# Optimization experiments

Measured on AMD Instinct MI355X. Metric: run time of the kernel, lower is better.

Reference implementation:

```python
import jax, jax.numpy as jnp
import numpy as np

B, S, D = 4, 2048, 1024      # batch, seq, d_model
H = 4096                     # expert hidden_size
E, K = 8, 2                  # num_experts, top_k
Z_COEF, BAL_COEF = 0.001, 0.01


def setup_inputs() -> dict:
    key = jax.random.key(0)
    ks = jax.random.split(key, 10)
    sc = 0.02
    return {
        "x": jax.random.normal(ks[0], (B, S, D), jnp.float32),
        "gate_w": jax.random.normal(ks[1], (D, E), jnp.float32) * sc,
        "keys_w": jax.random.normal(ks[2], (E, D, H), jnp.float32) * sc,
        "keys_b": jnp.zeros((E, H), jnp.float32),
        "values_w": jax.random.normal(ks[3], (E, H, D), jnp.float32) * sc,
        "values_b": jnp.zeros((E, D), jnp.float32),
        "shared_keys_w": jax.random.normal(ks[4], (D, H), jnp.float32) * sc,
        "shared_keys_b": jnp.zeros((H,), jnp.float32),
        "shared_values_w": jax.random.normal(ks[5], (H, D), jnp.float32) * sc,
        "shared_values_b": jnp.zeros((D,), jnp.float32),
    }


def reference(x, gate_w, keys_w, keys_b, values_w, values_b,
              shared_keys_w, shared_keys_b, shared_values_w, shared_values_b):
    b, s, d = x.shape
    xf = x.reshape(-1, d)                                  # [N, D]

    # ---- Router (top-k, softmax over selected scores) ----
    logits = xf @ gate_w                                   # [N, E]
    scores, idx = jax.lax.top_k(logits, K)                 # [N, K]
    w = jax.nn.softmax(scores, axis=-1)                    # [N, K]

    # Aux losses (training path)
    one_hot = jax.nn.one_hot(idx, E, dtype=w.dtype)        # [N, K, E]
    usage = (one_hot * w[..., None]).sum(axis=(0, 1))      # [E]
    balance_loss = usage.std() / usage.mean() * BAL_COEF
    z_loss = jnp.square(jax.nn.logsumexp(logits, axis=-1)).mean() * Z_COEF
    router_loss = balance_loss + z_loss

    # ---- Shared expert(s): single FFN, divided by count (=1) ----
    out = jax.nn.gelu(xf @ shared_keys_w + shared_keys_b) @ shared_values_w + shared_values_b

    # ---- Training path: dense per-expert FFN, masked combine ----
    # hidden: [N, E, H]
    hidden = jax.nn.gelu(jnp.einsum('nd,edh->neh', xf, keys_w) + keys_b)
    expert_out = jnp.einsum('neh,ehd->ned', hidden, values_w) + values_b  # [N, E, D]
    comb = (one_hot * w[..., None]).sum(axis=1)            # [N, E] per-token expert weight
    out = out + jnp.einsum('ned,ne->nd', expert_out, comb)

    return out.reshape(b, s, d), router_loss
```

## Files before the change

kernel.cpp:

```cpp
#include <hip/hip_runtime.h>
#include <hip/hip_bf16.h>


#define N_TOK 8192
#define DM    1024
#define HD    4096
#define NE    8
#define NKTOT 16384
#define PERM_CAP 17408
#define MAX_TILES 136
#define BAND 17
#define RTOK_BLK 16

typedef __attribute__((ext_vector_type(8))) short bhalf8;
typedef __attribute__((ext_vector_type(4))) float floatx4;

__device__ __forceinline__ unsigned short f2bf(float f) {
  union { float f; unsigned int u; } v; v.f = f;
  unsigned int u = v.u;
  return (unsigned short)((u + 0x7fffu + ((u >> 16) & 1u)) >> 16);
}

__device__ __forceinline__ float bf2f(unsigned short h) {
  union { unsigned int u; float f; } v; v.u = ((unsigned int)h) << 16;
  return v.f;
}

__device__ __forceinline__ float gelu_tanh(float h) {
  float u = 0.7978845608028654f * (h + 0.044715f * h * h * h);
  float t = 1.0f - 2.0f / (1.0f + __expf(2.0f * u));
  return 0.5f * h * (1.0f + t);
}

__device__ __forceinline__ void gload16(const unsigned short* g, void* l) {
  __builtin_amdgcn_global_load_lds(
      (const __attribute__((address_space(1))) void*)g,
      (__attribute__((address_space(3))) void*)l, 16, 0, 0);
}

__global__ void init_kernel(int* perm, float* permw, float* usage, float* zsum,
                            int* counts, int* fill) {
  int i = blockIdx.x * 256 + threadIdx.x;
  if (i < PERM_CAP) { perm[i] = 0; permw[i] = 0.0f; }
  if (i < NE) { usage[i] = 0.0f; counts[i] = 0; fill[i] = 0; }
  if (i == 0) zsum[0] = 0.0f;
}

__global__ void cvt_x_kernel(const float* __restrict__ x, unsigned short* __restrict__ xb) {
  size_t i = (size_t)(blockIdx.x * 256 + threadIdx.x) * 4;
  float4 v = *(const float4*)(x + i);
  ushort4 o;
  o.x = f2bf(v.x); o.y = f2bf(v.y); o.z = f2bf(v.z); o.w = f2bf(v.w);
  *(ushort4*)(xb + i) = o;
}

__global__ void router_kernel(const float* __restrict__ x, const float* __restrict__ gw,
                              int* __restrict__ idxb, float* __restrict__ wbuf,
                              float* __restrict__ usage, float* __restrict__ zsum,
                              int* __restrict__ counts) {
  __shared__ float s_use[NE];
  __shared__ int   s_cnt[NE];
  __shared__ float s_z;
  int t = threadIdx.x;
  if (t < NE) { s_use[t] = 0.0f; s_cnt[t] = 0; }
  if (t == 0) s_z = 0.0f;
  __syncthreads();

  int wave = t >> 6;
  int lane = t & 63;

  float luse[NE]; int lcnt[NE];
#pragma unroll
  for (int e = 0; e < NE; e++) { luse[e] = 0.0f; lcnt[e] = 0; }
  float lz = 0.0f;

#pragma unroll
  for (int i = 0; i < 4; i++) {
    int n = blockIdx.x * RTOK_BLK + wave * 4 + i;
    const float* xr = x + (size_t)n * DM;
    float acc[NE];
#pragma unroll
    for (int e = 0; e < NE; e++) acc[e] = 0.0f;
    for (int d = lane; d < DM; d += 64) {
      float xv = xr[d];
      const float* g = gw + (size_t)d * NE;
#pragma unroll
      for (int e = 0; e < NE; e++) acc[e] += xv * g[e];
    }
#pragma unroll
    for (int e = 0; e < NE; e++) {
#pragma unroll
      for (int off = 32; off > 0; off >>= 1) acc[e] += __shfl_xor(acc[e], off);
    }
    if (lane == 0) {
      float m1 = acc[0]; int i1 = 0;
#pragma unroll
      for (int e = 1; e < NE; e++) if (acc[e] > m1) { m1 = acc[e]; i1 = e; }
      float m2 = -3.0e38f; int i2 = 0;
#pragma unroll
      for (int e = 0; e < NE; e++) if (e != i1 && acc[e] > m2) { m2 = acc[e]; i2 = e; }
      float e1 = __expf(m2 - m1);
      float w1 = 1.0f / (1.0f + e1);
      float w2 = e1 / (1.0f + e1);
      float s = 0.0f;
#pragma unroll
      for (int e = 0; e < NE; e++) s += __expf(acc[e] - m1);
      float lse = m1 + __logf(s);
      idxb[n * 2 + 0] = i1; idxb[n * 2 + 1] = i2;
      wbuf[n * 2 + 0] = w1; wbuf[n * 2 + 1] = w2;
      luse[i1] += w1; luse[i2] += w2;
      lcnt[i1]++;     lcnt[i2]++;
      lz += lse * lse;
    }
  }

  if (lane == 0) {
#pragma unroll
    for (int e = 0; e < NE; e++) {
      atomicAdd(&s_use[e], luse[e]);
      atomicAdd(&s_cnt[e], lcnt[e]);
    }
    atomicAdd(&s_z, lz);
  }
  __syncthreads();
  if (t < NE) {
    atomicAdd(&usage[t], s_use[t]);
    atomicAdd(&counts[t], s_cnt[t]);
  }
  if (t == 0) atomicAdd(zsum, s_z);
}

__global__ void scan_kernel(const int* __restrict__ counts, int* __restrict__ poff,
                            int* __restrict__ tileE, int* __restrict__ tileR,
                            int* __restrict__ nTiles,
                            const float* __restrict__ usage, const float* __restrict__ zsum,
                            float* __restrict__ lossOut) {
  if (threadIdx.x == 0 && blockIdx.x == 0) {
    int run = 0, nt = 0;
    for (int e = 0; e < NE; e++) {
      poff[e] = run;
      int t = (counts[e] + 127) >> 7;
      for (int i = 0; i < t; i++) { tileE[nt] = e; tileR[nt] = run + i * 128; nt++; }
      run += t << 7;
    }
    *nTiles = nt;
    float mean = 0.0f;
    for (int e = 0; e < NE; e++) mean += usage[e];
    mean *= (1.0f / NE);
    float var = 0.0f;
    for (int e = 0; e < NE; e++) { float d = usage[e] - mean; var += d * d; }
    var *= (1.0f / NE);
    float bal = sqrtf(var) / mean * 0.01f;
    float z = (zsum[0] / (float)N_TOK) * 0.001f;
    lossOut[0] = bal + z;
  }
}

__global__ void scatter_kernel(const int* __restrict__ idxb, const float* __restrict__ wbuf,
                               const int* __restrict__ poff, int* __restrict__ fill,
                               int* __restrict__ perm, float* __restrict__ permw,
                               int* __restrict__ pos) {
  __shared__ int lcnt[NE];
  __shared__ int lbase[NE];
  int t = threadIdx.x;
  if (t < NE) lcnt[t] = 0;
  __syncthreads();
  int i = blockIdx.x * 256 + t;
  int e = idxb[i];
  int r = atomicAdd(&lcnt[e], 1);
  __syncthreads();
  if (t < NE) lbase[t] = atomicAdd(&fill[t], lcnt[t]);
  __syncthreads();
  int p = poff[e] + lbase[e] + r;
  perm[p] = i >> 1;
  permw[p] = wbuf[i];
  pos[i] = p;
}

__global__ void transpose_cvt_kernel(const float* __restrict__ src,
                                     unsigned short* __restrict__ dst, int R, int C) {
  __shared__ float tile[64][65];
  size_t bo = (size_t)blockIdx.z * R * C;
  src += bo; dst += bo;
  int r0 = blockIdx.x * 64, c0 = blockIdx.y * 64;
  int c = threadIdx.x & 63, r = threadIdx.x >> 6;
#pragma unroll
  for (int i = 0; i < 16; i++)
    tile[r + i * 4][c] = src[(size_t)(r0 + r + i * 4) * C + c0 + c];
  __syncthreads();
#pragma unroll
  for (int i = 0; i < 16; i++) {
    int oc = r + i * 4;
    float v = tile[c][oc];
    dst[(size_t)(c0 + oc) * R + r0 + c] = f2bf(v);
  }
}

__global__ void combine_kernel(float* __restrict__ out,
                               const unsigned short* __restrict__ eout,
                               const int* __restrict__ pos) {
  int t = blockIdx.x;
  int d = threadIdx.x * 8;
  int p0 = pos[t * 2], p1 = pos[t * 2 + 1];
  float* o = out + (size_t)t * DM + d;
  const unsigned short* e0 = eout + (size_t)p0 * DM + d;
  const unsigned short* e1 = eout + (size_t)p1 * DM + d;
  float4 a = *(const float4*)(o);
  float4 b = *(const float4*)(o + 4);
  ushort4 u0a = *(const ushort4*)(e0), u0b = *(const ushort4*)(e0 + 4);
  ushort4 u1a = *(const ushort4*)(e1), u1b = *(const ushort4*)(e1 + 4);
  a.x += bf2f(u0a.x) + bf2f(u1a.x);
  a.y += bf2f(u0a.y) + bf2f(u1a.y);
  a.z += bf2f(u0a.z) + bf2f(u1a.z);
  a.w += bf2f(u0a.w) + bf2f(u1a.w);
  b.x += bf2f(u0b.x) + bf2f(u1b.x);
  b.y += bf2f(u0b.y) + bf2f(u1b.y);
  b.z += bf2f(u0b.z) + bf2f(u1b.z);
  b.w += bf2f(u0b.w) + bf2f(u1b.w);
  *(float4*)(o) = a;
  *(float4*)(o + 4) = b;
}

template<int MODE>
__device__ __forceinline__ void gemm_body(
    const unsigned short* __restrict__ A,
    const unsigned short* __restrict__ BT,
    const float* __restrict__ bias,
    float* __restrict__ outF,
    unsigned short* __restrict__ outH,
    int Kd, int Nd,
    const int* __restrict__ perm,
    const float* __restrict__ permw,
    const int* __restrict__ tileE,
    const int* __restrict__ tileR,
    const int* __restrict__ nTiles) {
  __shared__ __align__(16) unsigned short As[128 * 64];
  __shared__ __align__(16) unsigned short Bs[128 * 64];

  int id = blockIdx.x;
  int xcd = id & 7, q = id >> 3;
  int mt, ntile;
  if (MODE == 0) {
    mt = xcd * 8 + (q & 7);
    ntile = q >> 3;
  } else if (MODE == 1) {
    ntile = q & 7;
    mt = xcd * 8 + (q >> 3);
  } else if (MODE == 2) {
    int n_in = q & 7, m_in = (q >> 3) & 3, ng = (q >> 5) & 3, mg = q >> 7;
    int mband = mg * 4 + m_in;
    if (mband >= BAND) return;
    mt = xcd * BAND + mband;
    ntile = ng * 8 + n_in;
  } else {
    mt = xcd * BAND + (q >> 3);
    ntile = q & 7;
  }

  int n0 = ntile * 128;
  int prow0 = 0, m0 = 0;
  if (MODE >= 2) {
    if (mt >= *nTiles) return;
    int e = tileE[mt];
    prow0 = tileR[mt];
    BT += (size_t)e * Kd * Nd;
    bias += (size_t)e * Nd;
  } else {
    m0 = mt * 128;
  }

  int t = threadIdx.x;
  int rsub = t >> 3;
  int gc = (t & 7) ^ (rsub & 7);
  const unsigned short* aptr[4];
  const unsigned short* bptr[4];
#pragma unroll
  for (int p = 0; p < 4; p++) {
    int r = rsub + p * 32;
    size_t grow;
    if (MODE == 2)      grow = (size_t)perm[prow0 + r];
    else if (MODE == 3) grow = (size_t)(prow0 + r);
    else                grow = (size_t)(m0 + r);
    aptr[p] = A + grow * Kd + gc * 8;
    bptr[p] = BT + (size_t)(n0 + r) * Kd + gc * 8;
  }
  char* ldsA = (char*)As + (t & 192) * 16;
  char* ldsB = (char*)Bs + (t & 192) * 16;

  int lane = t & 63;
  int wv = t >> 6;
  int wm = (wv >> 1) * 64, wn = (wv & 1) * 64;
  int lr = lane & 15, lq = lane >> 4;
  int rx = lr & 7;

  floatx4 acc[4][4];
#pragma unroll
  for (int i = 0; i < 4; i++)
#pragma unroll
    for (int j = 0; j < 4; j++) acc[i][j] = (floatx4){0.f, 0.f, 0.f, 0.f};

  for (int k0 = 0; k0 < Kd; k0 += 64) {
#pragma unroll
    for (int p = 0; p < 4; p++) {
      gload16(aptr[p] + k0, ldsA + p * 4096);
      gload16(bptr[p] + k0, ldsB + p * 4096);
    }
    __syncthreads();
#pragma unroll
    for (int kk = 0; kk < 2; kk++) {
      int ca = kk * 4 + lq;
      bhalf8 af[4], bf[4];
#pragma unroll
      for (int i = 0; i < 4; i++) {
        af[i] = *(const bhalf8*)&As[(wm + i * 16 + lr) * 64 + ((ca ^ rx) * 8)];
        bf[i] = *(const bhalf8*)&Bs[(wn + i * 16 + lr) * 64 + ((ca ^ rx) * 8)];
      }
#pragma unroll
      for (int mtile = 0; mtile < 4; mtile++)
#pragma unroll
        for (int ntl = 0; ntl < 4; ntl++)
          acc[mtile][ntl] = __builtin_amdgcn_mfma_f32_16x16x32_bf16(af[mtile], bf[ntl], acc[mtile][ntl], 0, 0, 0);
    }
    __syncthreads();
  }

#pragma unroll
  for (int mtile = 0; mtile < 4; mtile++) {
#pragma unroll
    for (int ntl = 0; ntl < 4; ntl++) {
      int ncol = n0 + wn + ntl * 16 + lr;
      float bb = bias[ncol];
#pragma unroll
      for (int r = 0; r < 4; r++) {
        int mrow = wm + mtile * 16 + lq * 4 + r;
        float v = acc[mtile][ntl][r] + bb;
        if (MODE == 0) {
          outH[(size_t)(m0 + mrow) * Nd + ncol] = f2bf(gelu_tanh(v));
        } else if (MODE == 1) {
          outF[(size_t)(m0 + mrow) * Nd + ncol] = v;
        } else if (MODE == 2) {
          outH[(size_t)(prow0 + mrow) * Nd + ncol] = f2bf(gelu_tanh(v));
        } else {
          int prow = prow0 + mrow;
          float w = permw[prow];
          outH[(size_t)prow * Nd + ncol] = f2bf(w * v);
        }
      }
    }
  }
}

__global__ __launch_bounds__(256, 4) void gemm_shared_keys(
    const unsigned short* A, const unsigned short* BT, const float* bias,
    float* outF, unsigned short* outH, int Kd, int Nd,
    const int* perm, const float* permw, const int* tE, const int* tR, const int* nT) {
  gemm_body<0>(A, BT, bias, outF, outH, Kd, Nd, perm, permw, tE, tR, nT);
}
__global__ __launch_bounds__(256, 4) void gemm_shared_values(
    const unsigned short* A, const unsigned short* BT, const float* bias,
    float* outF, unsigned short* outH, int Kd, int Nd,
    const int* perm, const float* permw, const int* tE, const int* tR, const int* nT) {
  gemm_body<1>(A, BT, bias, outF, outH, Kd, Nd, perm, permw, tE, tR, nT);
}
__global__ __launch_bounds__(256, 4) void gemm_expert_keys(
    const unsigned short* A, const unsigned short* BT, const float* bias,
    float* outF, unsigned short* outH, int Kd, int Nd,
    const int* perm, const float* permw, const int* tE, const int* tR, const int* nT) {
  gemm_body<2>(A, BT, bias, outF, outH, Kd, Nd, perm, permw, tE, tR, nT);
}
__global__ __launch_bounds__(256, 4) void gemm_expert_values(
    const unsigned short* A, const unsigned short* BT, const float* bias,
    float* outF, unsigned short* outH, int Kd, int Nd,
    const int* perm, const float* permw, const int* tE, const int* tR, const int* nT) {
  gemm_body<3>(A, BT, bias, outF, outH, Kd, Nd, perm, permw, tE, tR, nT);
}

extern "C" void kernel_launch(void* const* d_in, const int* in_sizes, int n_in,
                              void* d_out, int out_size, void* d_ws, size_t ws_size,
                              hipStream_t stream) {
  const float* x        = (const float*)d_in[0];
  const float* gate_w   = (const float*)d_in[1];
  const float* keys_w   = (const float*)d_in[2];
  const float* keys_b   = (const float*)d_in[3];
  const float* values_w = (const float*)d_in[4];
  const float* values_b = (const float*)d_in[5];
  const float* sk_w     = (const float*)d_in[6];
  const float* sk_b     = (const float*)d_in[7];
  const float* sv_w     = (const float*)d_in[8];
  const float* sv_b     = (const float*)d_in[9];
  float* out = (float*)d_out;

  char* p = (char*)d_ws;
  unsigned short* xb   = (unsigned short*)p; p += (size_t)N_TOK * DM * 2;
  unsigned short* wt   = (unsigned short*)p; p += (size_t)NE * DM * HD * 2;
  unsigned short* hid  = (unsigned short*)p; p += (size_t)PERM_CAP * HD * 2;
  unsigned short* eout = (unsigned short*)p; p += (size_t)PERM_CAP * DM * 2;
  int*   idxb   = (int*)p;   p += NKTOT * 4;
  float* wbuf   = (float*)p; p += NKTOT * 4;
  int*   perm   = (int*)p;   p += PERM_CAP * 4;
  float* permw  = (float*)p; p += PERM_CAP * 4;
  int*   pos    = (int*)p;   p += NKTOT * 4;
  int*   counts = (int*)p;   p += NE * 4;
  int*   fill   = (int*)p;   p += NE * 4;
  int*   poff   = (int*)p;   p += NE * 4;
  float* usage  = (float*)p; p += NE * 4;
  float* zsum   = (float*)p; p += 16;
  int*   tileE  = (int*)p;   p += MAX_TILES * 4;
  int*   tileR  = (int*)p;   p += MAX_TILES * 4;
  int*   nTiles = (int*)p;   p += 16;

  float* lossOut = out + (size_t)N_TOK * DM;

  init_kernel<<<(PERM_CAP + 255) / 256, 256, 0, stream>>>(perm, permw, usage, zsum, counts, fill);
  cvt_x_kernel<<<(N_TOK * DM / 4 + 255) / 256, 256, 0, stream>>>(x, xb);
  router_kernel<<<N_TOK / RTOK_BLK, 256, 0, stream>>>(x, gate_w, idxb, wbuf, usage, zsum, counts);
  scan_kernel<<<1, 64, 0, stream>>>(counts, poff, tileE, tileR, nTiles, usage, zsum, lossOut);
  scatter_kernel<<<NKTOT / 256, 256, 0, stream>>>(idxb, wbuf, poff, fill, perm, permw, pos);

  transpose_cvt_kernel<<<dim3(DM / 64, HD / 64, 1), 256, 0, stream>>>(sk_w, wt, DM, HD);
  gemm_shared_keys<<<2048, 256, 0, stream>>>(
      xb, wt, sk_b, nullptr, hid, DM, HD, perm, permw, tileE, tileR, nTiles);
  transpose_cvt_kernel<<<dim3(HD / 64, DM / 64, 1), 256, 0, stream>>>(sv_w, wt, HD, DM);
  gemm_shared_values<<<512, 256, 0, stream>>>(
      hid, wt, sv_b, out, nullptr, HD, DM, perm, permw, tileE, tileR, nTiles);

  transpose_cvt_kernel<<<dim3(DM / 64, HD / 64, NE), 256, 0, stream>>>(keys_w, wt, DM, HD);
  gemm_expert_keys<<<5120, 256, 0, stream>>>(
      xb, wt, keys_b, nullptr, hid, DM, HD, perm, permw, tileE, tileR, nTiles);
  transpose_cvt_kernel<<<dim3(HD / 64, DM / 64, NE), 256, 0, stream>>>(values_w, wt, HD, DM);
  gemm_expert_values<<<1088, 256, 0, stream>>>(
      hid, wt, values_b, nullptr, eout, HD, DM, perm, permw, tileE, tileR, nTiles);

  combine_kernel<<<N_TOK, 128, 0, stream>>>(out, eout, pos);
}
```

Baseline: 926.4 us.

## Fuse expert combine into values GEMM via atomics and vectorize transpose stores

The expert-values GEMM epilogue now atomically adds the weighted result straight into the fp32 output for each token. This removes the bf16 eout buffer and the separate combine kernel. The transpose kernel now writes 8 bf16 values per 16-byte vector store instead of scalar stores, and the values GEMM occupancy hint goes from 4 to 5 waves. Atomics add contention and non-deterministic summation order but cut one global round trip.

```diff
diff --git a/kernel.cpp b/kernel.cpp
--- a/kernel.cpp
+++ b/kernel.cpp
@@ -13,6 +13,7 @@
 #define RTOK_BLK 16
 
 typedef __attribute__((ext_vector_type(8))) short bhalf8;
+typedef __attribute__((ext_vector_type(8))) unsigned short ushort8v;
 typedef __attribute__((ext_vector_type(4))) float floatx4;
 
 __device__ __forceinline__ unsigned short f2bf(float f) {
@@ -188,37 +189,16 @@
   for (int i = 0; i < 16; i++)
     tile[r + i * 4][c] = src[(size_t)(r0 + r + i * 4) * C + c0 + c];
   __syncthreads();
-#pragma unroll
-  for (int i = 0; i < 16; i++) {
-    int oc = r + i * 4;
-    float v = tile[c][oc];
-    dst[(size_t)(c0 + oc) * R + r0 + c] = f2bf(v);
-  }
-}
-
-__global__ void combine_kernel(float* __restrict__ out,
-                               const unsigned short* __restrict__ eout,
-                               const int* __restrict__ pos) {
-  int t = blockIdx.x;
-  int d = threadIdx.x * 8;
-  int p0 = pos[t * 2], p1 = pos[t * 2 + 1];
-  float* o = out + (size_t)t * DM + d;
-  const unsigned short* e0 = eout + (size_t)p0 * DM + d;
-  const unsigned short* e1 = eout + (size_t)p1 * DM + d;
-  float4 a = *(const float4*)(o);
-  float4 b = *(const float4*)(o + 4);
-  ushort4 u0a = *(const ushort4*)(e0), u0b = *(const ushort4*)(e0 + 4);
-  ushort4 u1a = *(const ushort4*)(e1), u1b = *(const ushort4*)(e1 + 4);
-  a.x += bf2f(u0a.x) + bf2f(u1a.x);
-  a.y += bf2f(u0a.y) + bf2f(u1a.y);
-  a.z += bf2f(u0a.z) + bf2f(u1a.z);
-  a.w += bf2f(u0a.w) + bf2f(u1a.w);
-  b.x += bf2f(u0b.x) + bf2f(u1b.x);
-  b.y += bf2f(u0b.y) + bf2f(u1b.y);
-  b.z += bf2f(u0b.z) + bf2f(u1b.z);
-  b.w += bf2f(u0b.w) + bf2f(u1b.w);
-  *(float4*)(o) = a;
-  *(float4*)(o + 4) = b;
+  int u = threadIdx.x & 7;
+  int ow = threadIdx.x >> 3;
+#pragma unroll
+  for (int it = 0; it < 2; it++) {
+    int oc = ow + it * 32;
+    ushort8v o;
+#pragma unroll
+    for (int j = 0; j < 8; j++) o[j] = f2bf(tile[u * 8 + j][oc]);
+    *(ushort8v*)&dst[(size_t)(c0 + oc) * R + r0 + u * 8] = o;
+  }
 }
 
 template<int MODE>
@@ -343,7 +323,10 @@
         } else {
           int prow = prow0 + mrow;
           float w = permw[prow];
-          outH[(size_t)prow * Nd + ncol] = f2bf(w * v);
+          if (w != 0.0f) {
+            int tok = perm[prow];
+            atomicAdd(&outF[(size_t)tok * Nd + ncol], w * v);
+          }
         }
       }
     }
@@ -368,7 +351,7 @@
     const int* perm, const float* permw, const int* tE, const int* tR, const int* nT) {
   gemm_body<2>(A, BT, bias, outF, outH, Kd, Nd, perm, permw, tE, tR, nT);
 }
-__global__ __launch_bounds__(256, 4) void gemm_expert_values(
+__global__ __launch_bounds__(256, 5) void gemm_expert_values(
     const unsigned short* A, const unsigned short* BT, const float* bias,
     float* outF, unsigned short* outH, int Kd, int Nd,
     const int* perm, const float* permw, const int* tE, const int* tR, const int* nT) {
@@ -394,7 +377,6 @@
   unsigned short* xb   = (unsigned short*)p; p += (size_t)N_TOK * DM * 2;
   unsigned short* wt   = (unsigned short*)p; p += (size_t)NE * DM * HD * 2;
   unsigned short* hid  = (unsigned short*)p; p += (size_t)PERM_CAP * HD * 2;
-  unsigned short* eout = (unsigned short*)p; p += (size_t)PERM_CAP * DM * 2;
   int*   idxb   = (int*)p;   p += NKTOT * 4;
   float* wbuf   = (float*)p; p += NKTOT * 4;
   int*   perm   = (int*)p;   p += PERM_CAP * 4;
@@ -429,7 +411,5 @@
       xb, wt, keys_b, nullptr, hid, DM, HD, perm, permw, tileE, tileR, nTiles);
   transpose_cvt_kernel<<<dim3(HD / 64, DM / 64, NE), 256, 0, stream>>>(values_w, wt, HD, DM);
   gemm_expert_values<<<1088, 256, 0, stream>>>(
-      hid, wt, values_b, nullptr, eout, HD, DM, perm, permw, tileE, tileR, nTiles);
-
-  combine_kernel<<<N_TOK, 128, 0, stream>>>(out, eout, pos);
-}
+      hid, wt, values_b, out, nullptr, HD, DM, perm, permw, tileE, tileR, nTiles);
+}
```

Result: slower. 1.373 ms (+48.2%).
